# Kernel tuning notes

Hardware: AMD Instinct MI355X
Metric: run time of the kernel (lower is better)

## Reference

```python
import jax, jax.numpy as jnp
import numpy as np

B, LQ, LK, DK, DV = 32, 128, 4096, 256, 256


def setup_inputs() -> dict:
    key = jax.random.key(0)
    k1, k2, k3, k4, k5 = jax.random.split(key, 5)
    return {
        "query": jax.random.normal(k1, (B, LQ, DK), dtype=jnp.float32),
        "query_lengths": jax.random.randint(k2, (B,), 1, LQ, dtype=jnp.int32),
        "keys": jax.random.normal(k3, (B, LK, DK), dtype=jnp.float32),
        "values": jax.random.normal(k4, (B, LK, DV), dtype=jnp.float32),
        "mask": jax.random.randint(k5, (B, LK), 0, 2, dtype=jnp.int32),  # 1 = masked out
    }


def reference(query, query_lengths, keys, values, mask):
    # zero query positions beyond each example's length (torch: mask_query masked_fill 0)
    q_valid = jnp.arange(query.shape[1])[None, :] < query_lengths[:, None]  # [B, Lq]
    query = jnp.where(q_valid[:, :, None], query, 0.0)
    # zero masked key/value timesteps (torch mask: 1 -> masked)
    kv_valid = (mask == 0)[:, :, None]  # [B, Lk, 1]
    keys = jnp.where(kv_valid, keys, 0.0)
    values = jnp.where(kv_valid, values, 0.0)
    # attention scores [B, Lq, Lk]
    weights = jnp.einsum("bqd,bkd->bqk", query, keys)
    # exact-zero scores (masked rows/cols) -> -inf, matching torch weights==0.0 fill
    weights = jnp.where(weights == 0.0, -jnp.inf, weights)
    weights = jax.nn.softmax(weights, axis=-1)
    # rows that were all -inf produce NaN -> cleaned to 0
    weights = jnp.where(jnp.isnan(weights), 0.0, weights)
    attended = jnp.einsum("bqk,bkv->bqv", weights, values)  # [B, Lq, Dv]
    return jnp.mean(attended, axis=1)  # [B, Dv]
```

## Files before the change

kernel.cpp:

```cpp
#include <hip/hip_runtime.h>
#include <hip/hip_fp16.h>
#include <stdint.h>

#define NB  32
#define NLQ 128
#define NLK 4096
#define NDK 256
#define NDV 256
#define KT  16
#define SPLITS 8
#define MINSPLITS 4

typedef _Float16 f16;
typedef _Float16 f16x4 __attribute__((ext_vector_type(4)));
typedef _Float16 f16x8 __attribute__((ext_vector_type(8)));
typedef float    f32x4 __attribute__((ext_vector_type(4)));

__global__ __launch_bounds__(512) void fvta_part1(
    const float* __restrict__ q_, const float* __restrict__ k_,
    const float* __restrict__ v_, const int* __restrict__ mask_,
    f16* __restrict__ accw, float* __restrict__ mlw)
{
    __shared__ __align__(16) f16 KA[2][KT * NDK];
    __shared__ __align__(16) f16 QA[64 * NDK];
    __shared__ int MK[NLK / MINSPLITS];

    const int tid = threadIdx.x, w = tid >> 6, lane = tid & 63;
    const int l15 = lane & 15, lhi = lane >> 4;
    const int qsub = w >> 1;
    const int dvh  = w & 1;
    const int x = blockIdx.x, b = blockIdx.y;
    const int S = gridDim.x >> 1;
    const int s = x >> 1, qz = x & 1;
    const int slice = NLK / S, nt = slice / KT, kbase = s * slice;
    const float NEG = -__builtin_inff();

    const float* kb = k_ + ((size_t)b * NLK + kbase) * NDK;
    const float* vb = v_ + ((size_t)b * NLK + kbase) * NDV;
    const int*   mb = mask_ + b * NLK + kbase;

    for (int i = tid; i < slice; i += 512) MK[i] = mb[i];

    {
        const float* qsrc = q_ + ((size_t)b * NLQ + qz * 64) * NDK;
        #pragma unroll
        for (int r = 0; r < 8; ++r) {
            const int idx = r * 512 + tid;
            const int qq  = idx >> 6;
            const int d   = (idx & 63) * 4;
            f32x4 xv = *(const f32x4*)(qsrc + qq * NDK + d);
            f16x4 hh; hh[0]=(f16)xv[0]; hh[1]=(f16)xv[1]; hh[2]=(f16)xv[2]; hh[3]=(f16)xv[3];
            *(f16x4*)(QA + qq * NDK + (d ^ ((qq & 15) << 3))) = hh;
        }
    }

    f32x4 accu[8];
    #pragma unroll
    for (int i = 0; i < 8; ++i) accu[i] = (f32x4){0.f, 0.f, 0.f, 0.f};
    float m_run = NEG, l_run = 0.f;

    f32x4 ks[2];

    auto stage = [&](f16* KAb) {
        #pragma unroll
        for (int r = 0; r < 2; ++r) {
            const int idx = r * 512 + tid;
            const int kk  = idx >> 6;
            const int d   = (idx & 63) * 4;
            const int e   = kk * NDK + (d ^ (kk << 3));
            f32x4 xv = ks[r];
            f16x4 hh; hh[0]=(f16)xv[0]; hh[1]=(f16)xv[1]; hh[2]=(f16)xv[2]; hh[3]=(f16)xv[3];
            *(f16x4*)(KAb + e) = hh;
        }
    };

    #pragma unroll
    for (int r = 0; r < 2; ++r)
        ks[r] = *(const f32x4*)(kb + (r * 512 + tid) * 4);
    stage(KA[0]);
    __syncthreads();

    const int swz = l15 << 3;

    for (int t = 0; t < nt; ++t) {
        const int cur = t & 1;
        if (t + 1 < nt) {
            const float* ksrc = kb + (size_t)(t + 1) * KT * NDK;
            #pragma unroll
            for (int r = 0; r < 2; ++r)
                ks[r] = *(const f32x4*)(ksrc + (r * 512 + tid) * 4);
        }
        const int k0 = t * KT;

        f32x4 s4 = (f32x4){0.f,0.f,0.f,0.f};
        {
            const f16* kp = &KA[cur][l15 * NDK];
            const f16* qp = &QA[(qsub * 16 + l15) * NDK];
            #pragma unroll
            for (int kd = 0; kd < 8; ++kd) {
                const int col = (kd * 32 + lhi * 8) ^ swz;
                f16x8 kf = *(const f16x8*)(kp + col);
                f16x8 qv = *(const f16x8*)(qp + col);
                s4 = __builtin_amdgcn_mfma_f32_16x16x32_f16(kf, qv, s4, 0, 0, 0);
            }
        }

        const int4 m4 = *(const int4*)(MK + k0 + lhi * 4);
        float sa[4];
        sa[0] = m4.x ? NEG : s4[0]; sa[1] = m4.y ? NEG : s4[1];
        sa[2] = m4.z ? NEG : s4[2]; sa[3] = m4.w ? NEG : s4[3];

        float tmax = fmaxf(fmaxf(sa[0], sa[1]), fmaxf(sa[2], sa[3]));
        tmax = fmaxf(tmax, __shfl_xor(tmax, 16, 64));
        tmax = fmaxf(tmax, __shfl_xor(tmax, 32, 64));
        const float mnew = fmaxf(m_run, tmax);
        const bool  dead = (mnew == NEG);
        const float scale = dead ? 1.f : __expf(m_run - mnew);
        float p4[4];
        #pragma unroll
        for (int j = 0; j < 4; ++j) p4[j] = dead ? 0.f : __expf(sa[j] - mnew);
        float ps = (p4[0] + p4[1]) + (p4[2] + p4[3]);
        ps += __shfl_xor(ps, 16, 64);
        ps += __shfl_xor(ps, 32, 64);
        l_run = l_run * scale + ps;
        m_run = mnew;

        f16x4 pa;
        pa[0]=(f16)p4[0]; pa[1]=(f16)p4[1]; pa[2]=(f16)p4[2]; pa[3]=(f16)p4[3];

        if (!__all(scale == 1.f)) {
            float scj[4];
            #pragma unroll
            for (int j = 0; j < 4; ++j) scj[j] = __shfl(scale, lhi * 4 + j, 64);
            #pragma unroll
            for (int d = 0; d < 8; ++d) {
                accu[d][0] *= scj[0]; accu[d][1] *= scj[1];
                accu[d][2] *= scj[2]; accu[d][3] *= scj[3];
            }
        }

        {
            const float* vr = vb + (size_t)(k0 + lhi * 4) * NDV + dvh * 128 + l15;
            #pragma unroll
            for (int dg = 0; dg < 2; ++dg) {
                float tv[4][4];
                #pragma unroll
                for (int dd = 0; dd < 4; ++dd) {
                    const float* vc = vr + (dg * 4 + dd) * 16;
                    tv[dd][0] = vc[0];
                    tv[dd][1] = vc[1 * NDV];
                    tv[dd][2] = vc[2 * NDV];
                    tv[dd][3] = vc[3 * NDV];
                }
                #pragma unroll
                for (int dd = 0; dd < 4; ++dd) {
                    f16x4 vf;
                    vf[0]=(f16)tv[dd][0]; vf[1]=(f16)tv[dd][1];
                    vf[2]=(f16)tv[dd][2]; vf[3]=(f16)tv[dd][3];
                    accu[dg * 4 + dd] = __builtin_amdgcn_mfma_f32_16x16x16f16(
                        pa, vf, accu[dg * 4 + dd], 0, 0, 0);
                }
            }
        }

        if (t + 1 < nt) stage(KA[cur ^ 1]);
        __syncthreads();
    }

    const size_t base = (size_t)(b * S + s) * NLQ + qz * 64 + qsub * 16;
    #pragma unroll
    for (int j = 0; j < 4; ++j) {
        f16* dst = accw + (base + lhi * 4 + j) * NDV + dvh * 128 + l15;
        #pragma unroll
        for (int d = 0; d < 8; ++d) dst[d * 16] = (f16)accu[d][j];
    }
    if (dvh == 0 && lane < 16) {
        mlw[(base + lane) * 2]     = m_run;
        mlw[(base + lane) * 2 + 1] = l_run;
    }
}

__global__ __launch_bounds__(256) void fvta_merge(
    const f16* __restrict__ accw, const float* __restrict__ mlw,
    const int* __restrict__ qlen_, float* __restrict__ out_, int S)
{
    __shared__ float fac[8][SPLITS + 1];
    const int qc = blockIdx.x, b = blockIdx.y, tid = threadIdx.x;
    const int len = qlen_[b];
    const float NEG = -__builtin_inff();

    if (tid < 8) {
        const int q = qc * 8 + tid;
        if (q < len) {
            float gm = NEG;
            for (int ss = 0; ss < S; ++ss)
                gm = fmaxf(gm, mlw[((size_t)(b * S + ss) * NLQ + q) * 2]);
            float L = 0.f;
            for (int ss = 0; ss < S; ++ss) {
                const float m = mlw[((size_t)(b * S + ss) * NLQ + q) * 2];
                const float l = mlw[((size_t)(b * S + ss) * NLQ + q) * 2 + 1];
                if (m != NEG) L += l * __expf(m - gm);
            }
            for (int ss = 0; ss < S; ++ss) {
                const float m = mlw[((size_t)(b * S + ss) * NLQ + q) * 2];
                fac[tid][ss] = (gm != NEG && L > 0.f && m != NEG)
                             ? __expf(m - gm) / L : 0.f;
            }
        } else {
            for (int ss = 0; ss < S; ++ss) fac[tid][ss] = 0.f;
        }
    }
    __syncthreads();

    float sum = 0.f;
    for (int qq = 0; qq < 8; ++qq) {
        const int q = qc * 8 + qq;
        for (int ss = 0; ss < S; ++ss) {
            const float f = fac[qq][ss];
            if (f != 0.f)
                sum += (float)accw[((size_t)(b * S + ss) * NLQ + q) * NDV + tid] * f;
        }
    }
    atomicAdd(&out_[b * NDV + tid], sum * (1.f / NLQ));
}

extern "C" void kernel_launch(void* const* d_in, const int* in_sizes, int n_in,
                              void* d_out, int out_size, void* d_ws, size_t ws_size,
                              hipStream_t stream) {
    const float* q    = (const float*)d_in[0];
    const int*   qlen = (const int*)d_in[1];
    const float* k    = (const float*)d_in[2];
    const float* v    = (const float*)d_in[3];
    const int*   mask = (const int*)d_in[4];
    float* out = (float*)d_out;

    int S = SPLITS;
    while (S > MINSPLITS &&
           ((size_t)NB * S * NLQ * NDV * 2 + (size_t)NB * S * NLQ * 8) > ws_size)
        S >>= 1;
    f16*   accw = (f16*)d_ws;
    float* mlw  = (float*)((char*)d_ws + (size_t)NB * S * NLQ * NDV * 2);

    hipMemsetAsync(out, 0, (size_t)out_size * sizeof(float), stream);
    dim3 g1(2 * S, NB);
    fvta_part1<<<g1, 512, 0, stream>>>(q, k, v, mask, accw, mlw);
    dim3 g2(NLQ / 8, NB);
    fvta_merge<<<g2, 256, 0, stream>>>(accw, mlw, qlen, out, S);
}
```

Before: 124.6 us.

## Stage V tiles through double-buffered LDS and remap block-to-split ordering

Values are now prefetched with coalesced vector loads alongside K, converted to fp16 and written into a double-buffered swizzled shared-memory tile. The PV MFMA operands are then read from LDS instead of through strided scalar global loads, which each of the four q-subgroup waves had been repeating. The block index mapping is also changed so that, when S is 8, consecutive blocks cover different key splits instead of the two query halves of one split. This costs more LDS and registers, and the 2-byte scalar LDS reads may cause bank conflicts.

```diff
diff --git a/kernel.cpp b/kernel.cpp
--- a/kernel.cpp
+++ b/kernel.cpp
@@ -22,6 +22,7 @@
     f16* __restrict__ accw, float* __restrict__ mlw)
 {
     __shared__ __align__(16) f16 KA[2][KT * NDK];
+    __shared__ __align__(16) f16 VA[2][KT * NDV];
     __shared__ __align__(16) f16 QA[64 * NDK];
     __shared__ int MK[NLK / MINSPLITS];
 
@@ -31,7 +32,8 @@
     const int dvh  = w & 1;
     const int x = blockIdx.x, b = blockIdx.y;
     const int S = gridDim.x >> 1;
-    const int s = x >> 1, qz = x & 1;
+    const int s  = (S == 8) ? (x & 7) : (x >> 1);
+    const int qz = (S == 8) ? (x >> 3) : (x & 1);
     const int slice = NLK / S, nt = slice / KT, kbase = s * slice;
     const float NEG = -__builtin_inff();
 
@@ -59,9 +61,9 @@
     for (int i = 0; i < 8; ++i) accu[i] = (f32x4){0.f, 0.f, 0.f, 0.f};
     float m_run = NEG, l_run = 0.f;
 
-    f32x4 ks[2];
-
-    auto stage = [&](f16* KAb) {
+    f32x4 ks[2], vs[2];
+
+    auto stage = [&](f16* KAb, f16* VAb) {
         #pragma unroll
         for (int r = 0; r < 2; ++r) {
             const int idx = r * 512 + tid;
@@ -71,13 +73,18 @@
             f32x4 xv = ks[r];
             f16x4 hh; hh[0]=(f16)xv[0]; hh[1]=(f16)xv[1]; hh[2]=(f16)xv[2]; hh[3]=(f16)xv[3];
             *(f16x4*)(KAb + e) = hh;
+            f32x4 yv = vs[r];
+            f16x4 gg; gg[0]=(f16)yv[0]; gg[1]=(f16)yv[1]; gg[2]=(f16)yv[2]; gg[3]=(f16)yv[3];
+            *(f16x4*)(VAb + e) = gg;
         }
     };
 
     #pragma unroll
-    for (int r = 0; r < 2; ++r)
+    for (int r = 0; r < 2; ++r) {
         ks[r] = *(const f32x4*)(kb + (r * 512 + tid) * 4);
-    stage(KA[0]);
+        vs[r] = *(const f32x4*)(vb + (r * 512 + tid) * 4);
+    }
+    stage(KA[0], VA[0]);
     __syncthreads();
 
     const int swz = l15 << 3;
@@ -86,9 +93,12 @@
         const int cur = t & 1;
         if (t + 1 < nt) {
             const float* ksrc = kb + (size_t)(t + 1) * KT * NDK;
-            #pragma unroll
-            for (int r = 0; r < 2; ++r)
+            const float* vsrc = vb + (size_t)(t + 1) * KT * NDV;
+            #pragma unroll
+            for (int r = 0; r < 2; ++r) {
                 ks[r] = *(const f32x4*)(ksrc + (r * 512 + tid) * 4);
+                vs[r] = *(const f32x4*)(vsrc + (r * 512 + tid) * 4);
+            }
         }
         const int k0 = t * KT;
 
@@ -140,30 +150,26 @@
         }
 
         {
-            const float* vr = vb + (size_t)(k0 + lhi * 4) * NDV + dvh * 128 + l15;
+            const f16* VL = &VA[cur][0];
             #pragma unroll
             for (int dg = 0; dg < 2; ++dg) {
-                float tv[4][4];
-                #pragma unroll
-                for (int dd = 0; dd < 4; ++dd) {
-                    const float* vc = vr + (dg * 4 + dd) * 16;
-                    tv[dd][0] = vc[0];
-                    tv[dd][1] = vc[1 * NDV];
-                    tv[dd][2] = vc[2 * NDV];
-                    tv[dd][3] = vc[3 * NDV];
-                }
                 #pragma unroll
                 for (int dd = 0; dd < 4; ++dd) {
                     f16x4 vf;
-                    vf[0]=(f16)tv[dd][0]; vf[1]=(f16)tv[dd][1];
-                    vf[2]=(f16)tv[dd][2]; vf[3]=(f16)tv[dd][3];
+                    #pragma unroll
+                    for (int j = 0; j < 4; ++j) {
+                        const int rr  = lhi * 4 + j;
+                        const int col = (dvh * 128 + (dg * 4 + dd) * 16 + l15)
+                                        ^ (rr << 3);
+                        vf[j] = VL[rr * NDV + col];
+                    }
                     accu[dg * 4 + dd] = __builtin_amdgcn_mfma_f32_16x16x16f16(
                         pa, vf, accu[dg * 4 + dd], 0, 0, 0);
                 }
             }
         }
 
-        if (t + 1 < nt) stage(KA[cur ^ 1]);
+        if (t + 1 < nt) stage(KA[cur ^ 1], VA[cur ^ 1]);
         __syncthreads();
     }
 
```

Measured after the change: 128.3 us. 1.03x slower.

## Double key tile, defer softmax rescaling, normalize partials before fp16 store

Applied to the files above, without the earlier changes.

Raises the key tile from 16 to 32 rows, so each iteration runs two score MFMAs per k-slice and two PV passes, halving barrier and loop overhead. Adds lazy max rescaling: the running max and accumulator are only updated when some lane's tile max exceeds the current max by more than 8, which skips the rescale shuffles and multiplies most of the time. Partial accumulators are divided by l before the fp16 store to avoid overflow from the deferred max, and the merge now weights each split by l. This costs more registers, and p values up to about e^8 in fp16 may lose some precision.

```diff
diff --git a/kernel.cpp b/kernel.cpp
--- a/kernel.cpp
+++ b/kernel.cpp
@@ -7,7 +7,7 @@
 #define NLK 4096
 #define NDK 256
 #define NDV 256
-#define KT  16
+#define KT  32
 #define SPLITS 8
 #define MINSPLITS 4
 
@@ -59,15 +59,15 @@
     for (int i = 0; i < 8; ++i) accu[i] = (f32x4){0.f, 0.f, 0.f, 0.f};
     float m_run = NEG, l_run = 0.f;
 
-    f32x4 ks[2];
+    f32x4 ks[4];
 
     auto stage = [&](f16* KAb) {
         #pragma unroll
-        for (int r = 0; r < 2; ++r) {
+        for (int r = 0; r < 4; ++r) {
             const int idx = r * 512 + tid;
             const int kk  = idx >> 6;
             const int d   = (idx & 63) * 4;
-            const int e   = kk * NDK + (d ^ (kk << 3));
+            const int e   = kk * NDK + (d ^ ((kk & 15) << 3));
             f32x4 xv = ks[r];
             f16x4 hh; hh[0]=(f16)xv[0]; hh[1]=(f16)xv[1]; hh[2]=(f16)xv[2]; hh[3]=(f16)xv[3];
             *(f16x4*)(KAb + e) = hh;
@@ -75,7 +75,7 @@
     };
 
     #pragma unroll
-    for (int r = 0; r < 2; ++r)
+    for (int r = 0; r < 4; ++r)
         ks[r] = *(const f32x4*)(kb + (r * 512 + tid) * 4);
     stage(KA[0]);
     __syncthreads();
@@ -87,78 +87,104 @@
         if (t + 1 < nt) {
             const float* ksrc = kb + (size_t)(t + 1) * KT * NDK;
             #pragma unroll
-            for (int r = 0; r < 2; ++r)
+            for (int r = 0; r < 4; ++r)
                 ks[r] = *(const f32x4*)(ksrc + (r * 512 + tid) * 4);
         }
         const int k0 = t * KT;
 
-        f32x4 s4 = (f32x4){0.f,0.f,0.f,0.f};
+        f32x4 s4a = (f32x4){0.f,0.f,0.f,0.f}, s4b = s4a;
         {
-            const f16* kp = &KA[cur][l15 * NDK];
-            const f16* qp = &QA[(qsub * 16 + l15) * NDK];
+            const f16* k0p = &KA[cur][(0 * 16 + l15) * NDK];
+            const f16* k1p = &KA[cur][(1 * 16 + l15) * NDK];
+            const f16* qp  = &QA[(qsub * 16 + l15) * NDK];
             #pragma unroll
             for (int kd = 0; kd < 8; ++kd) {
                 const int col = (kd * 32 + lhi * 8) ^ swz;
-                f16x8 kf = *(const f16x8*)(kp + col);
-                f16x8 qv = *(const f16x8*)(qp + col);
-                s4 = __builtin_amdgcn_mfma_f32_16x16x32_f16(kf, qv, s4, 0, 0, 0);
-            }
-        }
-
-        const int4 m4 = *(const int4*)(MK + k0 + lhi * 4);
-        float sa[4];
-        sa[0] = m4.x ? NEG : s4[0]; sa[1] = m4.y ? NEG : s4[1];
-        sa[2] = m4.z ? NEG : s4[2]; sa[3] = m4.w ? NEG : s4[3];
-
-        float tmax = fmaxf(fmaxf(sa[0], sa[1]), fmaxf(sa[2], sa[3]));
+                f16x8 qv  = *(const f16x8*)(qp + col);
+                f16x8 kfa = *(const f16x8*)(k0p + col);
+                s4a = __builtin_amdgcn_mfma_f32_16x16x32_f16(kfa, qv, s4a, 0, 0, 0);
+                f16x8 kfb = *(const f16x8*)(k1p + col);
+                s4b = __builtin_amdgcn_mfma_f32_16x16x32_f16(kfb, qv, s4b, 0, 0, 0);
+            }
+        }
+
+        const int4 m4a = *(const int4*)(MK + k0 + lhi * 4);
+        const int4 m4b = *(const int4*)(MK + k0 + 16 + lhi * 4);
+        float sa[4], sb[4];
+        sa[0] = m4a.x ? NEG : s4a[0]; sa[1] = m4a.y ? NEG : s4a[1];
+        sa[2] = m4a.z ? NEG : s4a[2]; sa[3] = m4a.w ? NEG : s4a[3];
+        sb[0] = m4b.x ? NEG : s4b[0]; sb[1] = m4b.y ? NEG : s4b[1];
+        sb[2] = m4b.z ? NEG : s4b[2]; sb[3] = m4b.w ? NEG : s4b[3];
+
+        float tmax = fmaxf(fmaxf(fmaxf(sa[0], sa[1]), fmaxf(sa[2], sa[3])),
+                           fmaxf(fmaxf(sb[0], sb[1]), fmaxf(sb[2], sb[3])));
         tmax = fmaxf(tmax, __shfl_xor(tmax, 16, 64));
         tmax = fmaxf(tmax, __shfl_xor(tmax, 32, 64));
-        const float mnew = fmaxf(m_run, tmax);
-        const bool  dead = (mnew == NEG);
-        const float scale = dead ? 1.f : __expf(m_run - mnew);
-        float p4[4];
-        #pragma unroll
-        for (int j = 0; j < 4; ++j) p4[j] = dead ? 0.f : __expf(sa[j] - mnew);
-        float ps = (p4[0] + p4[1]) + (p4[2] + p4[3]);
+
+        const bool defer = (m_run != NEG) && __all(tmax - m_run <= 8.f);
+        if (!defer) {
+            const float mnew = fmaxf(m_run, tmax);
+            if (mnew != NEG) {
+                const float scale = (m_run == NEG) ? 0.f : __expf(m_run - mnew);
+                float scj[4];
+                #pragma unroll
+                for (int j = 0; j < 4; ++j) scj[j] = __shfl(scale, lhi * 4 + j, 64);
+                #pragma unroll
+                for (int d = 0; d < 8; ++d) {
+                    accu[d][0] *= scj[0]; accu[d][1] *= scj[1];
+                    accu[d][2] *= scj[2]; accu[d][3] *= scj[3];
+                }
+                l_run *= scale;
+                m_run = mnew;
+            }
+        }
+
+        float p4a[4], p4b[4];
+        if (m_run == NEG) {
+            #pragma unroll
+            for (int j = 0; j < 4; ++j) { p4a[j] = 0.f; p4b[j] = 0.f; }
+        } else {
+            #pragma unroll
+            for (int j = 0; j < 4; ++j) {
+                p4a[j] = __expf(sa[j] - m_run);
+                p4b[j] = __expf(sb[j] - m_run);
+            }
+        }
+        float ps = (p4a[0] + p4a[1]) + (p4a[2] + p4a[3])
+                 + (p4b[0] + p4b[1]) + (p4b[2] + p4b[3]);
         ps += __shfl_xor(ps, 16, 64);
         ps += __shfl_xor(ps, 32, 64);
-        l_run = l_run * scale + ps;
-        m_run = mnew;
-
-        f16x4 pa;
-        pa[0]=(f16)p4[0]; pa[1]=(f16)p4[1]; pa[2]=(f16)p4[2]; pa[3]=(f16)p4[3];
-
-        if (!__all(scale == 1.f)) {
-            float scj[4];
-            #pragma unroll
-            for (int j = 0; j < 4; ++j) scj[j] = __shfl(scale, lhi * 4 + j, 64);
-            #pragma unroll
-            for (int d = 0; d < 8; ++d) {
-                accu[d][0] *= scj[0]; accu[d][1] *= scj[1];
-                accu[d][2] *= scj[2]; accu[d][3] *= scj[3];
-            }
-        }
+        l_run += ps;
+
+        f16x4 pa, pb;
+        pa[0]=(f16)p4a[0]; pa[1]=(f16)p4a[1]; pa[2]=(f16)p4a[2]; pa[3]=(f16)p4a[3];
+        pb[0]=(f16)p4b[0]; pb[1]=(f16)p4b[1]; pb[2]=(f16)p4b[2]; pb[3]=(f16)p4b[3];
 
         {
-            const float* vr = vb + (size_t)(k0 + lhi * 4) * NDV + dvh * 128 + l15;
-            #pragma unroll
-            for (int dg = 0; dg < 2; ++dg) {
-                float tv[4][4];
+            #pragma unroll
+            for (int h = 0; h < 2; ++h) {
+                const f16x4 pfrag = h ? pb : pa;
+                const float* vr = vb + (size_t)(k0 + h * 16 + lhi * 4) * NDV
+                                + dvh * 128 + l15;
                 #pragma unroll
-                for (int dd = 0; dd < 4; ++dd) {
-                    const float* vc = vr + (dg * 4 + dd) * 16;
-                    tv[dd][0] = vc[0];
-                    tv[dd][1] = vc[1 * NDV];
-                    tv[dd][2] = vc[2 * NDV];
-                    tv[dd][3] = vc[3 * NDV];
-                }
-                #pragma unroll
-                for (int dd = 0; dd < 4; ++dd) {
-                    f16x4 vf;
-                    vf[0]=(f16)tv[dd][0]; vf[1]=(f16)tv[dd][1];
-                    vf[2]=(f16)tv[dd][2]; vf[3]=(f16)tv[dd][3];
-                    accu[dg * 4 + dd] = __builtin_amdgcn_mfma_f32_16x16x16f16(
-                        pa, vf, accu[dg * 4 + dd], 0, 0, 0);
+                for (int dg = 0; dg < 2; ++dg) {
+                    float tv[4][4];
+                    #pragma unroll
+                    for (int dd = 0; dd < 4; ++dd) {
+                        const float* vc = vr + (dg * 4 + dd) * 16;
+                        tv[dd][0] = vc[0];
+                        tv[dd][1] = vc[1 * NDV];
+                        tv[dd][2] = vc[2 * NDV];
+                        tv[dd][3] = vc[3 * NDV];
+                    }
+                    #pragma unroll
+                    for (int dd = 0; dd < 4; ++dd) {
+                        f16x4 vf;
+                        vf[0]=(f16)tv[dd][0]; vf[1]=(f16)tv[dd][1];
+                        vf[2]=(f16)tv[dd][2]; vf[3]=(f16)tv[dd][3];
+                        accu[dg * 4 + dd] = __builtin_amdgcn_mfma_f32_16x16x16f16(
+                            pfrag, vf, accu[dg * 4 + dd], 0, 0, 0);
+                    }
                 }
             }
         }
@@ -166,13 +192,18 @@
         if (t + 1 < nt) stage(KA[cur ^ 1]);
         __syncthreads();
     }
+
+    const float rl = (l_run > 0.f) ? 1.f / l_run : 0.f;
+    float rlj[4];
+    #pragma unroll
+    for (int j = 0; j < 4; ++j) rlj[j] = __shfl(rl, lhi * 4 + j, 64);
 
     const size_t base = (size_t)(b * S + s) * NLQ + qz * 64 + qsub * 16;
     #pragma unroll
     for (int j = 0; j < 4; ++j) {
         f16* dst = accw + (base + lhi * 4 + j) * NDV + dvh * 128 + l15;
         #pragma unroll
-        for (int d = 0; d < 8; ++d) dst[d * 16] = (f16)accu[d][j];
+        for (int d = 0; d < 8; ++d) dst[d * 16] = (f16)(accu[d][j] * rlj[j]);
     }
     if (dvh == 0 && lane < 16) {
         mlw[(base + lane) * 2]     = m_run;
@@ -203,8 +234,9 @@
             }
             for (int ss = 0; ss < S; ++ss) {
                 const float m = mlw[((size_t)(b * S + ss) * NLQ + q) * 2];
+                const float l = mlw[((size_t)(b * S + ss) * NLQ + q) * 2 + 1];
                 fac[tid][ss] = (gm != NEG && L > 0.f && m != NEG)
-                             ? __expf(m - gm) / L : 0.f;
+                             ? l * __expf(m - gm) / L : 0.f;
             }
         } else {
             for (int ss = 0; ss < S; ++ss) fac[tid][ss] = 0.f;
```

Result: slower. 127.4 us (+2.3%).
